# Performance work log

Measured on AMD Instinct MI355X. Metric: run time of the kernel, lower is better.

Reference implementation:

```python
import jax, jax.numpy as jnp
import numpy as np

T, N, H, D = 128, 2048, 128, 128  # timesteps, envs, hidden_dim, embedding_dim
EPS = 1e-5


def layer_norm(x, w, b):
    m = x.mean(-1, keepdims=True)
    v = ((x - m) ** 2).mean(-1, keepdims=True)
    return (x - m) * jax.lax.rsqrt(v + EPS) * w + b


def setup_inputs() -> dict:
    key = jax.random.key(0)
    ks = jax.random.split(key, 10)
    s = 0.05
    return {
        "x": jax.random.normal(ks[0], (T * N, D), jnp.float32),
        "hxs": jax.random.normal(ks[1], (N, 1, H), jnp.float32),
        "masks": jax.random.randint(ks[2], (T * N, 1), 0, 2).astype(jnp.float32),
        "ln1_w": jnp.ones((D,), jnp.float32),
        "ln1_b": jnp.zeros((D,), jnp.float32),
        "W1": jax.random.normal(ks[3], (H, D), jnp.float32) * s,
        "b1": jnp.zeros((H,), jnp.float32),
        "W2": jax.random.normal(ks[4], (H, H), jnp.float32) * s,
        "b2": jnp.zeros((H,), jnp.float32),
        "W_ih": jax.random.normal(ks[5], (3 * H, H), jnp.float32) * s,
        "b_ih": jnp.zeros((3 * H,), jnp.float32),
        "W_hh": jax.random.normal(ks[6], (3 * H, H), jnp.float32) * s,
        "b_hh": jnp.zeros((3 * H,), jnp.float32),
        "ln2_w": jnp.ones((H,), jnp.float32),
        "ln2_b": jnp.zeros((H,), jnp.float32),
    }


def reference(x, hxs, masks, ln1_w, ln1_b, W1, b1, W2, b2,
              W_ih, b_ih, W_hh, b_hh, ln2_w, ln2_b):
    # feature norm + two linear layers (no nonlinearity in the original)
    feats = layer_norm(x, ln1_w, ln1_b)            # [T*N, D]
    feats = feats @ W1.T + b1                      # [T*N, H]
    feats = feats @ W2.T + b2                      # [T*N, H]
    feats = feats.reshape(T, N, H)
    m = masks.reshape(T, N)

    # precompute input-side GRU gates once (big GEMM outside the scan)
    gi = feats @ W_ih.T + b_ih                     # [T, N, 3H]

    h0 = hxs[:, 0, :]                              # num_rnn_layers == 1

    def step(h, inp):
        gi_t, m_t = inp
        h = h * m_t[:, None]                       # mask-reset (== segment split)
        gh = h @ W_hh.T + b_hh                     # [N, 3H]
        i_r, i_z, i_n = jnp.split(gi_t, 3, axis=-1)
        h_r, h_z, h_n = jnp.split(gh, 3, axis=-1)
        r = jax.nn.sigmoid(i_r + h_r)
        z = jax.nn.sigmoid(i_z + h_z)
        n = jnp.tanh(i_n + r * h_n)
        h_new = (1.0 - z) * n + z * h
        return h_new, h_new

    hT, outs = jax.lax.scan(step, h0, (gi, m))     # outs: [T, N, H]

    out = layer_norm(outs.reshape(T * N, H), ln2_w, ln2_b)
    return out, hT[:, None, :]
```

## Files before the change

### kernel.cpp

```cpp
#include <hip/hip_runtime.h>
#include <hip/hip_bf16.h>

#define Tt 128
#define Nn 2048
#define Hh 128
#define Dd 128
#define NB 8
#define LDA 136
#define LDG 388

typedef __attribute__((ext_vector_type(8))) short v8s;
typedef __attribute__((ext_vector_type(4))) float v4f;

__device__ __forceinline__ unsigned short f2bf(float f) {
    unsigned int u = __builtin_bit_cast(unsigned int, f);
    u += 0x7FFFu + ((u >> 16) & 1u);
    return (unsigned short)(u >> 16);
}

__device__ __forceinline__ v4f mfma_bf(v8s a, v8s b, v4f c) {
    return __builtin_amdgcn_mfma_f32_16x16x32_bf16(a, b, c, 0, 0, 0);
}

__device__ __forceinline__ v8s load_wfrag_bf(const float* __restrict__ W, int row, int k0) {
    const v4f* p = (const v4f*)(W + row * 128 + k0);
    v4f a = p[0], b = p[1];
    v8s r;
    r[0] = (short)f2bf(a[0]); r[1] = (short)f2bf(a[1]);
    r[2] = (short)f2bf(a[2]); r[3] = (short)f2bf(a[3]);
    r[4] = (short)f2bf(b[0]); r[5] = (short)f2bf(b[1]);
    r[6] = (short)f2bf(b[2]); r[7] = (short)f2bf(b[3]);
    return r;
}

__device__ __forceinline__ void store_bf4(unsigned short* p, v4f v) {
    unsigned int lo = ((unsigned int)f2bf(v[1]) << 16) | (unsigned int)f2bf(v[0]);
    unsigned int hi = ((unsigned int)f2bf(v[3]) << 16) | (unsigned int)f2bf(v[2]);
    uint2 d; d.x = lo; d.y = hi;
    *(uint2*)p = d;
}

__device__ __forceinline__ float sigm(float x) { return __frcp_rn(1.f + __expf(-x)); }
__device__ __forceinline__ float tanh_f(float x) {
    return 2.f * __frcp_rn(1.f + __expf(-2.f * x)) - 1.f;
}

__global__ __launch_bounds__(512, 2)
void rppo_pipe(const float* __restrict__ x, const float* __restrict__ hxs,
               const float* __restrict__ masks,
               const float* __restrict__ ln1_w, const float* __restrict__ ln1_b,
               const float* __restrict__ W1, const float* __restrict__ b1,
               const float* __restrict__ W2, const float* __restrict__ b2,
               const float* __restrict__ Wih, const float* __restrict__ bih,
               const float* __restrict__ Whh, const float* __restrict__ bhh,
               const float* __restrict__ ln2_w, const float* __restrict__ ln2_b,
               float* __restrict__ out)
{
    __shared__ unsigned short fbuf[16 * LDA];
    __shared__ unsigned short abuf[16 * LDA];
    __shared__ unsigned short bbuf[16 * LDA];
    __shared__ unsigned short hbuf[16 * LDA];
    __shared__ float gibuf[8 * LDG];
    __shared__ float ghbuf[8 * LDG];
    __shared__ float mbuf[Tt * NB];

    const int tid  = threadIdx.x;
    const int wave = tid >> 6;
    const int lane = tid & 63;
    const int l16  = lane & 15;
    const int quad = lane >> 4;
    const int arow = l16 & 7;
    const int wsub = wave & 3;
    const bool isP = (wave < 4);
    const int n0   = blockIdx.x * NB;

    v8s wreg[10][4];
    float brA[2], brB[2], brC[6];
    if (isP) {
#pragma unroll
        for (int c = 0; c < 2; ++c) {
            int rowc = (2 * wsub + c) * 16 + l16;
            brA[c] = b1[rowc];
            brB[c] = b2[rowc];
#pragma unroll
            for (int kk = 0; kk < 4; ++kk) {
                int k0 = kk * 32 + quad * 8;
                wreg[c][kk]     = load_wfrag_bf(W1, rowc, k0);
                wreg[2 + c][kk] = load_wfrag_bf(W2, rowc, k0);
            }
        }
#pragma unroll
        for (int c = 0; c < 6; ++c) {
            int rowc = (6 * wsub + c) * 16 + l16;
            brC[c] = bih[rowc];
#pragma unroll
            for (int kk = 0; kk < 4; ++kk)
                wreg[4 + c][kk] = load_wfrag_bf(Wih, rowc, kk * 32 + quad * 8);
        }
    } else {
#pragma unroll
        for (int c = 0; c < 6; ++c) {
            int rowc = (6 * wsub + c) * 16 + l16;
            brC[c] = bhh[rowc];
#pragma unroll
            for (int kk = 0; kk < 4; ++kk)
                wreg[4 + c][kk] = load_wfrag_bf(Whh, rowc, kk * 32 + quad * 8);
        }
    }

    for (int i = tid; i < Tt * NB; i += 512) {
        int t = i >> 3, b = i & 7;
        mbuf[i] = masks[t * Nn + n0 + b];
    }

    const int col4 = (tid & 31) << 2;
    const int row8 = tid >> 5;
    const int prow = (wave - 4) * 2 + (lane >> 5);

    v4f ln1w, ln1b, ln2w, ln2b, h, xv;
    if (isP) {
        ln1w = *(const v4f*)(ln1_w + col4);
        ln1b = *(const v4f*)(ln1_b + col4);
        xv = *(const v4f*)(x + (size_t)(n0 + row8) * Dd + col4);
    } else {
        ln2w = *(const v4f*)(ln2_w + col4);
        ln2b = *(const v4f*)(ln2_b + col4);
        h = *(const v4f*)(hxs + (size_t)(n0 + prow) * Hh + col4);
        h *= masks[n0 + prow];
        store_bf4(hbuf + prow * LDA + col4, h);
    }
    __syncthreads();

    for (int i = 0; i <= Tt; ++i) {
        if (isP) {
            if (i < Tt) {
                float s  = xv[0] + xv[1] + xv[2] + xv[3];
                float ss = xv[0]*xv[0] + xv[1]*xv[1] + xv[2]*xv[2] + xv[3]*xv[3];
#pragma unroll
                for (int m = 1; m < 32; m <<= 1) {
                    s  += __shfl_xor(s,  m, 64);
                    ss += __shfl_xor(ss, m, 64);
                }
                float mu = s * (1.f / 128.f);
                float rs = __frsqrt_rn(ss * (1.f / 128.f) - mu * mu + 1e-5f);
                v4f f;
#pragma unroll
                for (int e = 0; e < 4; ++e) f[e] = (xv[e] - mu) * rs * ln1w[e] + ln1b[e];
                store_bf4(fbuf + row8 * LDA + col4, f);
                if (i + 1 < Tt)
                    xv = *(const v4f*)(x + ((size_t)(i + 1) * Nn + n0 + row8) * Dd + col4);
            }
        } else if (i >= 1) {
            const int t = i - 1;
            const float* gb = gibuf + prow * LDG + col4;
            const float* hb = ghbuf + prow * LDG + col4;
            v4f ir  = *(const v4f*)(gb);
            v4f iz  = *(const v4f*)(gb + 128);
            v4f inn = *(const v4f*)(gb + 256);
            v4f hr  = *(const v4f*)(hb);
            v4f hz  = *(const v4f*)(hb + 128);
            v4f hn  = *(const v4f*)(hb + 256);
            v4f hnew;
#pragma unroll
            for (int e = 0; e < 4; ++e) {
                float r = sigm(ir[e] + hr[e]);
                float z = sigm(iz[e] + hz[e]);
                float n = tanh_f(inn[e] + r * hn[e]);
                hnew[e] = n + z * (h[e] - n);
            }
            float s2  = hnew[0] + hnew[1] + hnew[2] + hnew[3];
            float ss2 = hnew[0]*hnew[0] + hnew[1]*hnew[1] + hnew[2]*hnew[2] + hnew[3]*hnew[3];
#pragma unroll
            for (int m = 1; m < 32; m <<= 1) {
                s2  += __shfl_xor(s2,  m, 64);
                ss2 += __shfl_xor(ss2, m, 64);
            }
            float mu2 = s2 * (1.f / 128.f);
            float rs2 = __frsqrt_rn(ss2 * (1.f / 128.f) - mu2 * mu2 + 1e-5f);
            v4f o;
#pragma unroll
            for (int e = 0; e < 4; ++e) o[e] = (hnew[e] - mu2) * rs2 * ln2w[e] + ln2b[e];
            *(v4f*)(out + ((size_t)t * Nn + n0 + prow) * Hh + col4) = o;

            if (t + 1 < Tt) {
                float mt = mbuf[(t + 1) * NB + prow];
                h = hnew * mt;
                store_bf4(hbuf + prow * LDA + col4, h);
            } else {
                *(v4f*)(out + (size_t)Tt * Nn * Hh + (size_t)(n0 + prow) * Hh + col4) = hnew;
            }
        }
        __syncthreads();

        if (isP && i < Tt) {
            v8s af[4];
#pragma unroll
            for (int kk = 0; kk < 4; ++kk)
                af[kk] = *(const v8s*)(fbuf + arow * LDA + kk * 32 + quad * 8);
            v4f acc[2] = {{0.f,0.f,0.f,0.f},{0.f,0.f,0.f,0.f}};
#pragma unroll
            for (int c = 0; c < 2; ++c)
#pragma unroll
                for (int kk = 0; kk < 4; ++kk)
                    acc[c] = mfma_bf(af[kk], wreg[c][kk], acc[c]);
#pragma unroll
            for (int c = 0; c < 2; ++c) {
                int col = (2 * wsub + c) * 16 + l16;
#pragma unroll
                for (int rr = 0; rr < 4; ++rr) {
                    int row = quad * 4 + rr;
                    if (row < 8) abuf[row * LDA + col] = f2bf(acc[c][rr] + brA[c]);
                }
            }
        }
        __syncthreads();

        if (isP && i < Tt) {
            v8s af[4];
#pragma unroll
            for (int kk = 0; kk < 4; ++kk)
                af[kk] = *(const v8s*)(abuf + arow * LDA + kk * 32 + quad * 8);
            v4f acc[2] = {{0.f,0.f,0.f,0.f},{0.f,0.f,0.f,0.f}};
#pragma unroll
            for (int c = 0; c < 2; ++c)
#pragma unroll
                for (int kk = 0; kk < 4; ++kk)
                    acc[c] = mfma_bf(af[kk], wreg[2 + c][kk], acc[c]);
#pragma unroll
            for (int c = 0; c < 2; ++c) {
                int col = (2 * wsub + c) * 16 + l16;
#pragma unroll
                for (int rr = 0; rr < 4; ++rr) {
                    int row = quad * 4 + rr;
                    if (row < 8) bbuf[row * LDA + col] = f2bf(acc[c][rr] + brB[c]);
                }
            }
        }
        __syncthreads();

        if (i < Tt) {
            const unsigned short* srcA = isP ? bbuf : hbuf;
            float* dst = isP ? gibuf : ghbuf;
            v8s af[4];
#pragma unroll
            for (int kk = 0; kk < 4; ++kk)
                af[kk] = *(const v8s*)(srcA + arow * LDA + kk * 32 + quad * 8);
            v4f acc[6];
#pragma unroll
            for (int c = 0; c < 6; ++c) acc[c] = (v4f){0.f,0.f,0.f,0.f};
#pragma unroll
            for (int c = 0; c < 6; ++c)
#pragma unroll
                for (int kk = 0; kk < 4; ++kk)
                    acc[c] = mfma_bf(af[kk], wreg[4 + c][kk], acc[c]);
#pragma unroll
            for (int c = 0; c < 6; ++c) {
                int col = (6 * wsub + c) * 16 + l16;
#pragma unroll
                for (int rr = 0; rr < 4; ++rr) {
                    int row = quad * 4 + rr;
                    if (row < 8) dst[row * LDG + col] = acc[c][rr] + brC[c];
                }
            }
        }
        __syncthreads();
    }
}

extern "C" void kernel_launch(void* const* d_in, const int* in_sizes, int n_in,
                              void* d_out, int out_size, void* d_ws, size_t ws_size,
                              hipStream_t stream) {
    const float* x     = (const float*)d_in[0];
    const float* hxs   = (const float*)d_in[1];
    const float* masks = (const float*)d_in[2];
    const float* ln1w  = (const float*)d_in[3];
    const float* ln1b  = (const float*)d_in[4];
    const float* W1    = (const float*)d_in[5];
    const float* b1    = (const float*)d_in[6];
    const float* W2    = (const float*)d_in[7];
    const float* b2    = (const float*)d_in[8];
    const float* Wih   = (const float*)d_in[9];
    const float* bih   = (const float*)d_in[10];
    const float* Whh   = (const float*)d_in[11];
    const float* bhh   = (const float*)d_in[12];
    const float* ln2w  = (const float*)d_in[13];
    const float* ln2b  = (const float*)d_in[14];
    float* out = (float*)d_out;

    hipLaunchKernelGGL(rppo_pipe, dim3(Nn / NB), dim3(512), 0, stream,
                       x, hxs, masks, ln1w, ln1b, W1, b1, W2, b2,
                       Wih, bih, Whh, bhh, ln2w, ln2b, out);
}
```

Before: 573.4 us.

## Split W1/W2 GEMMs across wave groups with a double-buffered stage

The producer waves now do only the W1 GEMM, and the W2 GEMM moves to the recurrent waves, which were idle in that phase. A double-buffered intermediate buffer lets the two run one timestep apart. This removes one barrier-separated phase per step (four syncs become three), at the cost of one extra pipeline iteration and a deeper skew between stages. Weight registers drop from 10 to 8 fragment sets per wave and the shared buffers shrink to 8 rows, which lowers register and LDS pressure.

```diff
diff --git a/kernel.cpp b/kernel.cpp
--- a/kernel.cpp
+++ b/kernel.cpp
@@ -45,21 +45,21 @@
     return 2.f * __frcp_rn(1.f + __expf(-2.f * x)) - 1.f;
 }
 
-__global__ __launch_bounds__(512, 2)
-void rppo_pipe(const float* __restrict__ x, const float* __restrict__ hxs,
-               const float* __restrict__ masks,
-               const float* __restrict__ ln1_w, const float* __restrict__ ln1_b,
-               const float* __restrict__ W1, const float* __restrict__ b1,
-               const float* __restrict__ W2, const float* __restrict__ b2,
-               const float* __restrict__ Wih, const float* __restrict__ bih,
-               const float* __restrict__ Whh, const float* __restrict__ bhh,
-               const float* __restrict__ ln2_w, const float* __restrict__ ln2_b,
-               float* __restrict__ out)
+__global__ __launch_bounds__(512) __attribute__((amdgpu_waves_per_eu(2, 2)))
+void rppo_pipe2(const float* __restrict__ x, const float* __restrict__ hxs,
+                const float* __restrict__ masks,
+                const float* __restrict__ ln1_w, const float* __restrict__ ln1_b,
+                const float* __restrict__ W1, const float* __restrict__ b1,
+                const float* __restrict__ W2, const float* __restrict__ b2,
+                const float* __restrict__ Wih, const float* __restrict__ bih,
+                const float* __restrict__ Whh, const float* __restrict__ bhh,
+                const float* __restrict__ ln2_w, const float* __restrict__ ln2_b,
+                float* __restrict__ out)
 {
-    __shared__ unsigned short fbuf[16 * LDA];
-    __shared__ unsigned short abuf[16 * LDA];
-    __shared__ unsigned short bbuf[16 * LDA];
-    __shared__ unsigned short hbuf[16 * LDA];
+    __shared__ unsigned short fbuf[8 * LDA];
+    __shared__ unsigned short abuf[2][8 * LDA];
+    __shared__ unsigned short bbuf[8 * LDA];
+    __shared__ unsigned short hbuf[8 * LDA];
     __shared__ float gibuf[8 * LDG];
     __shared__ float ghbuf[8 * LDG];
     __shared__ float mbuf[Tt * NB];
@@ -74,37 +74,28 @@
     const bool isP = (wave < 4);
     const int n0   = blockIdx.x * NB;
 
-    v8s wreg[10][4];
-    float brA[2], brB[2], brC[6];
-    if (isP) {
+    v8s wreg[8][4];
+    float brAB[2], brC[6];
+    {
+        const float* Wab = isP ? W1 : W2;
+        const float* bab = isP ? b1 : b2;
+        const float* Wc  = isP ? Wih : Whh;
+        const float* bc  = isP ? bih : bhh;
 #pragma unroll
         for (int c = 0; c < 2; ++c) {
             int rowc = (2 * wsub + c) * 16 + l16;
-            brA[c] = b1[rowc];
-            brB[c] = b2[rowc];
-#pragma unroll
-            for (int kk = 0; kk < 4; ++kk) {
-                int k0 = kk * 32 + quad * 8;
-                wreg[c][kk]     = load_wfrag_bf(W1, rowc, k0);
-                wreg[2 + c][kk] = load_wfrag_bf(W2, rowc, k0);
-            }
+            brAB[c] = bab[rowc];
+#pragma unroll
+            for (int kk = 0; kk < 4; ++kk)
+                wreg[c][kk] = load_wfrag_bf(Wab, rowc, kk * 32 + quad * 8);
         }
 #pragma unroll
         for (int c = 0; c < 6; ++c) {
             int rowc = (6 * wsub + c) * 16 + l16;
-            brC[c] = bih[rowc];
+            brC[c] = bc[rowc];
 #pragma unroll
             for (int kk = 0; kk < 4; ++kk)
-                wreg[4 + c][kk] = load_wfrag_bf(Wih, rowc, kk * 32 + quad * 8);
-        }
-    } else {
-#pragma unroll
-        for (int c = 0; c < 6; ++c) {
-            int rowc = (6 * wsub + c) * 16 + l16;
-            brC[c] = bhh[rowc];
-#pragma unroll
-            for (int kk = 0; kk < 4; ++kk)
-                wreg[4 + c][kk] = load_wfrag_bf(Whh, rowc, kk * 32 + quad * 8);
+                wreg[2 + c][kk] = load_wfrag_bf(Wc, rowc, kk * 32 + quad * 8);
         }
     }
 
@@ -131,7 +122,7 @@
     }
     __syncthreads();
 
-    for (int i = 0; i <= Tt; ++i) {
+    for (int i = 0; i <= Tt + 1; ++i) {
         if (isP) {
             if (i < Tt) {
                 float s  = xv[0] + xv[1] + xv[2] + xv[3];
@@ -150,8 +141,8 @@
                 if (i + 1 < Tt)
                     xv = *(const v4f*)(x + ((size_t)(i + 1) * Nn + n0 + row8) * Dd + col4);
             }
-        } else if (i >= 1) {
-            const int t = i - 1;
+        } else if (i >= 2) {
+            const int t = i - 2;
             const float* gb = gibuf + prow * LDG + col4;
             const float* hb = ghbuf + prow * LDG + col4;
             v4f ir  = *(const v4f*)(gb);
@@ -192,67 +183,49 @@
         }
         __syncthreads();
 
-        if (isP && i < Tt) {
+        {
+            const bool act = isP ? (i < Tt) : (i >= 1 && i <= Tt);
+            if (act) {
+                const unsigned short* src = isP ? fbuf : abuf[(i + 1) & 1];
+                unsigned short* dst = isP ? abuf[i & 1] : bbuf;
+                v8s af[4];
+#pragma unroll
+                for (int kk = 0; kk < 4; ++kk)
+                    af[kk] = *(const v8s*)(src + arow * LDA + kk * 32 + quad * 8);
+                v4f acc[2] = {{0.f,0.f,0.f,0.f},{0.f,0.f,0.f,0.f}};
+#pragma unroll
+                for (int c = 0; c < 2; ++c)
+#pragma unroll
+                    for (int kk = 0; kk < 4; ++kk)
+                        acc[c] = mfma_bf(af[kk], wreg[c][kk], acc[c]);
+#pragma unroll
+                for (int c = 0; c < 2; ++c) {
+                    int col = (2 * wsub + c) * 16 + l16;
+#pragma unroll
+                    for (int rr = 0; rr < 4; ++rr) {
+                        int row = quad * 4 + rr;
+                        if (row < 8) dst[row * LDA + col] = f2bf(acc[c][rr] + brAB[c]);
+                    }
+                }
+            }
+        }
+        __syncthreads();
+
+        if (i >= 1 && i <= Tt) {
+            const unsigned short* src = isP ? bbuf : hbuf;
+            float* dst = isP ? gibuf : ghbuf;
             v8s af[4];
 #pragma unroll
             for (int kk = 0; kk < 4; ++kk)
-                af[kk] = *(const v8s*)(fbuf + arow * LDA + kk * 32 + quad * 8);
-            v4f acc[2] = {{0.f,0.f,0.f,0.f},{0.f,0.f,0.f,0.f}};
-#pragma unroll
-            for (int c = 0; c < 2; ++c)
-#pragma unroll
-                for (int kk = 0; kk < 4; ++kk)
-                    acc[c] = mfma_bf(af[kk], wreg[c][kk], acc[c]);
-#pragma unroll
-            for (int c = 0; c < 2; ++c) {
-                int col = (2 * wsub + c) * 16 + l16;
-#pragma unroll
-                for (int rr = 0; rr < 4; ++rr) {
-                    int row = quad * 4 + rr;
-                    if (row < 8) abuf[row * LDA + col] = f2bf(acc[c][rr] + brA[c]);
-                }
-            }
-        }
-        __syncthreads();
-
-        if (isP && i < Tt) {
-            v8s af[4];
-#pragma unroll
-            for (int kk = 0; kk < 4; ++kk)
-                af[kk] = *(const v8s*)(abuf + arow * LDA + kk * 32 + quad * 8);
-            v4f acc[2] = {{0.f,0.f,0.f,0.f},{0.f,0.f,0.f,0.f}};
-#pragma unroll
-            for (int c = 0; c < 2; ++c)
+                af[kk] = *(const v8s*)(src + arow * LDA + kk * 32 + quad * 8);
+            v4f acc[6];
+#pragma unroll
+            for (int c = 0; c < 6; ++c) acc[c] = (v4f){0.f,0.f,0.f,0.f};
+#pragma unroll
+            for (int c = 0; c < 6; ++c)
 #pragma unroll
                 for (int kk = 0; kk < 4; ++kk)
                     acc[c] = mfma_bf(af[kk], wreg[2 + c][kk], acc[c]);
-#pragma unroll
-            for (int c = 0; c < 2; ++c) {
-                int col = (2 * wsub + c) * 16 + l16;
-#pragma unroll
-                for (int rr = 0; rr < 4; ++rr) {
-                    int row = quad * 4 + rr;
-                    if (row < 8) bbuf[row * LDA + col] = f2bf(acc[c][rr] + brB[c]);
-                }
-            }
-        }
-        __syncthreads();
-
-        if (i < Tt) {
-            const unsigned short* srcA = isP ? bbuf : hbuf;
-            float* dst = isP ? gibuf : ghbuf;
-            v8s af[4];
-#pragma unroll
-            for (int kk = 0; kk < 4; ++kk)
-                af[kk] = *(const v8s*)(srcA + arow * LDA + kk * 32 + quad * 8);
-            v4f acc[6];
-#pragma unroll
-            for (int c = 0; c < 6; ++c) acc[c] = (v4f){0.f,0.f,0.f,0.f};
-#pragma unroll
-            for (int c = 0; c < 6; ++c)
-#pragma unroll
-                for (int kk = 0; kk < 4; ++kk)
-                    acc[c] = mfma_bf(af[kk], wreg[4 + c][kk], acc[c]);
 #pragma unroll
             for (int c = 0; c < 6; ++c) {
                 int col = (6 * wsub + c) * 16 + l16;
@@ -287,7 +260,7 @@
     const float* ln2b  = (const float*)d_in[14];
     float* out = (float*)d_out;
 
-    hipLaunchKernelGGL(rppo_pipe, dim3(Nn / NB), dim3(512), 0, stream,
+    hipLaunchKernelGGL(rppo_pipe2, dim3(Nn / NB), dim3(512), 0, stream,
                        x, hxs, masks, ln1w, ln1b, W1, b1, W2, b2,
                        Wih, bih, Whh, bhh, ln2w, ln2b, out);
 }
```

New measurement: 628.8 us. 1.1x slower.
